# Optimization experiments

Hardware: AMD Instinct MI355X
Metric: run time of the kernel (lower is better)

## Reference

```python
import jax, jax.numpy as jnp
import numpy as np

H = 8          # num_heads (in_channels > 8)
BN_EPS = 1e-5  # torch BatchNorm2d default


def _l2norm(w):
    # torch.norm(w, 2, dim=-2, keepdim=True) + 1e-4
    return jnp.sqrt(jnp.sum(w * w, axis=-2, keepdims=True)) + 1e-4


def setup_inputs() -> dict:
    key = jax.random.key(0)
    ks = jax.random.split(key, 6)
    N, C, T, V = 64, 128, 128, 25
    x = jax.random.normal(ks[0], (N, C, T, V), dtype=jnp.float32)
    fc1 = jax.random.normal(ks[1], (3, H, V, V), dtype=jnp.float32)
    rpe = jax.random.normal(ks[2], (3, H, V), dtype=jnp.float32)
    hops = jax.random.randint(ks[3], (V, V), 0, V)
    fc2_w = jax.random.normal(ks[4], (3, C, C // H), dtype=jnp.float32) * 0.1
    fc2_b = jax.random.normal(ks[5], (3, C), dtype=jnp.float32) * 0.1
    gamma = jnp.ones((C,), dtype=jnp.float32)
    beta = jnp.zeros((C,), dtype=jnp.float32)
    return {"x": x, "fc1": fc1, "rpe": rpe, "hops": hops,
            "fc2_w": fc2_w, "fc2_b": fc2_b, "gamma": gamma, "beta": beta}


def reference(x, fc1, rpe, hops, fc2_w, fc2_b, gamma, beta):
    N, C, T, V = x.shape
    c = C // H
    # relative-position embedding gathered by hop distance: (3, H, V, V)
    pos_emb = rpe[:, :, hops]
    x_in = x.reshape(N, H, c, T, V)
    y = jnp.zeros((N, H, c, T, V), dtype=x.dtype)
    for i in range(3):
        # normalized adaptive adjacency + normalized positional term
        w1 = fc1[i] / _l2norm(fc1[i]) + pos_emb[i] / _l2norm(pos_emb[i])  # (H, V, V)
        z = jnp.einsum('nhctv,hvw->nhctw', x_in, w1)
        # grouped 1x1 conv == per-head channel mixing
        wg = fc2_w[i].reshape(H, c, c)                       # (H, out_per_group, in_per_group)
        z = jnp.einsum('nhctv,hdc->nhdtv', z, wg)
        z = z + fc2_b[i].reshape(1, H, c, 1, 1)
        y = y + z
    y = y.reshape(N, C, T, V)
    # BatchNorm2d (training-mode batch statistics, biased variance)
    mean = jnp.mean(y, axis=(0, 2, 3), keepdims=True)
    var = jnp.var(y, axis=(0, 2, 3), keepdims=True)
    y = gamma.reshape(1, C, 1, 1) * (y - mean) * jax.lax.rsqrt(var + BN_EPS) + beta.reshape(1, C, 1, 1)
    # residual (in_channels == out_channels -> identity down) + ReLU
    return jax.nn.relu(y + x)
```

## Files before the change

### kernel.cpp

```cpp
#include <hip/hip_runtime.h>
#include <hip/hip_bf16.h>

namespace {

constexpr int kN = 64, kC = 128, kT = 128, kV = 25, kH = 8, kc = 16;
constexpr int kKS = 13;
constexpr int kBCol = 448;
constexpr int kBStep = kBCol * 32;
constexpr int kXRow = 424;

typedef __attribute__((ext_vector_type(8))) short bf16x8;
typedef __attribute__((ext_vector_type(8))) unsigned short u16x8;
typedef __attribute__((ext_vector_type(4))) float f32x4;

__device__ inline unsigned short f2bf(float f) {
    unsigned int u = __builtin_bit_cast(unsigned int, f);
    u += 0x7fffu + ((u >> 16) & 1u);
    return (unsigned short)(u >> 16);
}

__device__ inline float bf2f(unsigned short s) {
    return __builtin_bit_cast(float, ((unsigned int)s) << 16);
}

__device__ inline void glds16(const void* g, void* l) {
    __builtin_amdgcn_global_load_lds(
        (const __attribute__((address_space(1))) void*)g,
        (__attribute__((address_space(3))) void*)l, 16, 0, 0);
}
__device__ inline void glds4(const void* g, void* l) {
    __builtin_amdgcn_global_load_lds(
        (const __attribute__((address_space(1))) void*)g,
        (__attribute__((address_space(3))) void*)l, 4, 0, 0);
}

#define VMWAIT(n) do { asm volatile("s_waitcnt vmcnt(" #n ")" ::: "memory"); \
                       __builtin_amdgcn_sched_barrier(0); } while (0)
#define LGKM0     do { asm volatile("s_waitcnt lgkmcnt(0)" ::: "memory"); \
                       __builtin_amdgcn_sched_barrier(0); } while (0)
#define BAR()     __builtin_amdgcn_s_barrier()

__global__ void precompute_w1(const float* __restrict__ fc1,
                              const float* __restrict__ rpe,
                              const int* __restrict__ hops,
                              float* __restrict__ W1) {
    int ih = blockIdx.x;
    int w = threadIdx.x;
    if (w >= kV) return;
    const float* f = fc1 + ih * kV * kV;
    const float* r = rpe + ih * kV;
    float s1 = 0.f, s2 = 0.f;
    for (int v = 0; v < kV; ++v) {
        float a = f[v * kV + w];
        float p = r[hops[v * kV + w]];
        s1 += a * a; s2 += p * p;
    }
    float n1 = sqrtf(s1) + 1e-4f, n2 = sqrtf(s2) + 1e-4f;
    float* o = W1 + ih * kV * kV;
    for (int v = 0; v < kV; ++v) {
        float a = f[v * kV + w];
        float p = r[hops[v * kV + w]];
        o[v * kV + w] = a / n1 + p / n2;
    }
}

__global__ void precompute_W(const float* __restrict__ W1,
                             const float* __restrict__ fc2_w,
                             unsigned short* __restrict__ Wt3) {
    int k = blockIdx.x;
    int h = blockIdx.y;
    unsigned short* outp = Wt3 + ((size_t)h * kKS + k) * kBStep;
    for (int e = threadIdx.x; e < kBStep; e += 256) {
        int col = e >> 5, lo = e & 31;
        int kap = k * 32 + lo;
        int c = kap / 26, vv = kap - c * 26;
        float val = 0.f;
        if (vv < 25 && col < 400) {
            int d = col / 25, w = col - d * 25;
            #pragma unroll
            for (int i = 0; i < 3; ++i) {
                float wg = fc2_w[(i * kC + h * kc + d) * kc + c];
                float w1 = W1[((i * kH + h) * kV + vv) * kV + w];
                val += wg * w1;
            }
        }
        outp[e] = f2bf(val);
    }
}

__global__ __launch_bounds__(256, 1) void gemm_y(const float* __restrict__ x,
                                                 const unsigned short* __restrict__ Wt3,
                                                 unsigned short* __restrict__ yb) {
    __shared__ __align__(16) unsigned short Xl[64 * kXRow];
    __shared__ __align__(16) unsigned short Bl[2][kBStep];

    const int n = blockIdx.x, tb = blockIdx.y, h = blockIdx.z;
    const int tid = threadIdx.x, lane = tid & 63, wv = tid >> 6;
    const int ll = lane & 15, lh = lane >> 4;
    const int t0 = tb * 64;

    const float* xbase = x + ((size_t)(n * kC + h * kc) * kT + t0) * kV;
    const unsigned short* bbase = Wt3 + (size_t)h * kKS * kBStep;

    auto stage_x = [&](int s, int buf) {
        float* bb = (float*)&Bl[buf][0];
        const float* src0 = xbase + (size_t)(s * 4) * (kT * kV);
        #pragma unroll
        for (int q = 0; q < 25; ++q) {
            int e = q * 256 + tid;
            int c = e / 1600, off = e - c * 1600;
            glds4(src0 + (size_t)c * (kT * kV) + off, bb + e);
        }
    };
    auto convert = [&](int s, int buf) {
        const float* bp = (const float*)&Bl[buf][0] + (tid & 3) * 1600 + (tid >> 2) * 25;
        unsigned int* xw = (unsigned int*)&Xl[(size_t)(tid >> 2) * kXRow + (s * 4 + (tid & 3)) * 26];
        #pragma unroll
        for (int p = 0; p < 13; ++p) {
            float f0 = bp[2 * p];
            float f1 = (p < 12) ? bp[2 * p + 1] : 0.f;
            xw[p] = (unsigned)f2bf(f0) | ((unsigned)f2bf(f1) << 16);
        }
    };
    auto stage_b = [&](int k, int buf) {
        const unsigned short* src = bbase + (size_t)k * kBStep;
        unsigned short* dst = &Bl[buf][0];
        #pragma unroll
        for (int q = 0; q < 7; ++q)
            glds16(src + (size_t)(q * 256 + tid) * 8, dst + (size_t)(q * 256 + tid) * 8);
    };

    stage_x(0, 0); stage_x(1, 1);
    VMWAIT(25); BAR();
    convert(0, 0);
    LGKM0; BAR();
    stage_x(2, 0);
    VMWAIT(25); BAR();
    convert(1, 1);
    LGKM0; BAR();
    stage_x(3, 1);
    VMWAIT(25); BAR();
    convert(2, 0);
    LGKM0; BAR();
    stage_b(0, 0);
    VMWAIT(7); BAR();
    convert(3, 1);
    LGKM0; BAR();

    f32x4 acc[4][7];
    #pragma unroll
    for (int a = 0; a < 4; ++a)
        #pragma unroll
        for (int b = 0; b < 7; ++b) acc[a][b] = (f32x4)(0.f);

    for (int k = 0; k < kKS; ++k) {
        const int cur = k & 1;
        if (k < kKS - 1) {
            stage_b(k + 1, cur ^ 1);
            VMWAIT(7);
        } else {
            VMWAIT(0);
        }
        BAR();

        bf16x8 af0 = *(const bf16x8*)&Xl[(size_t)((0 * 16 + ll) * kXRow) + k * 32 + lh * 8];
        bf16x8 af1 = *(const bf16x8*)&Xl[(size_t)((1 * 16 + ll) * kXRow) + k * 32 + lh * 8];
        bf16x8 af2 = *(const bf16x8*)&Xl[(size_t)((2 * 16 + ll) * kXRow) + k * 32 + lh * 8];
        bf16x8 af3 = *(const bf16x8*)&Xl[(size_t)((3 * 16 + ll) * kXRow) + k * 32 + lh * 8];
        #pragma unroll
        for (int ci = 0; ci < 7; ++ci) {
            bf16x8 bf = *(const bf16x8*)&Bl[cur][(size_t)(((wv * 7 + ci) * 16 + ll) * 32) + lh * 8];
            acc[0][ci] = __builtin_amdgcn_mfma_f32_16x16x32_bf16(af0, bf, acc[0][ci], 0, 0, 0);
            acc[1][ci] = __builtin_amdgcn_mfma_f32_16x16x32_bf16(af1, bf, acc[1][ci], 0, 0, 0);
            acc[2][ci] = __builtin_amdgcn_mfma_f32_16x16x32_bf16(af2, bf, acc[2][ci], 0, 0, 0);
            acc[3][ci] = __builtin_amdgcn_mfma_f32_16x16x32_bf16(af3, bf, acc[3][ci], 0, 0, 0);
        }
        BAR();
    }

    #pragma unroll
    for (int rf = 0; rf < 4; ++rf) {
        int t = t0 + rf * 16 + lh * 4;
        #pragma unroll
        for (int ci = 0; ci < 7; ++ci) {
            int m = (wv * 7 + ci) * 16 + ll;
            if (m < 400) {
                int d = m / 25, w = m - d * 25;
                unsigned short* yp = yb + ((size_t)(n * kC + h * kc + d) * kT + t) * kV + w;
                #pragma unroll
                for (int r = 0; r < 4; ++r)
                    yp[(size_t)r * kV] = f2bf(acc[rf][ci][r]);
            }
        }
    }
}

__global__ void bn_partial(const unsigned short* __restrict__ yb,
                           float2* __restrict__ partials) {
    int g  = blockIdx.x;
    int ch = blockIdx.y;
    int tid = threadIdx.x;
    float s = 0.f, ss = 0.f;
    for (int n = g * 8; n < g * 8 + 8; ++n) {
        const u16x8* p = (const u16x8*)(yb + (size_t)(n * kC + ch) * (kT * kV));
        for (int e = tid; e < 400; e += 256) {
            u16x8 v = p[e];
            #pragma unroll
            for (int j = 0; j < 8; ++j) {
                float f = bf2f((unsigned short)v[j]);
                s += f; ss += f * f;
            }
        }
    }
    __shared__ float rs[256], rss[256];
    rs[tid] = s; rss[tid] = ss;
    __syncthreads();
    for (int o = 128; o > 0; o >>= 1) {
        if (tid < o) { rs[tid] += rs[tid + o]; rss[tid] += rss[tid + o]; }
        __syncthreads();
    }
    if (tid == 0) partials[ch * 8 + g] = make_float2(rs[0], rss[0]);
}

__global__ void bn_finalize(const float2* __restrict__ partials,
                            const float* __restrict__ gamma,
                            const float* __restrict__ beta,
                            float2* __restrict__ scsh) {
    int ch = threadIdx.x;
    if (ch >= kC) return;
    float s = 0.f, ss = 0.f;
    for (int g = 0; g < 8; ++g) {
        float2 p = partials[ch * 8 + g];
        s += p.x; ss += p.y;
    }
    const float inv = 1.f / (float)(kN * kT * kV);
    float mean = s * inv;
    float var  = ss * inv - mean * mean;
    float sc = gamma[ch] * rsqrtf(var + 1e-5f);
    scsh[ch] = make_float2(sc, beta[ch] - mean * sc);
}

__global__ void bn_apply(const unsigned short* __restrict__ yb,
                         const float* __restrict__ x,
                         const float2* __restrict__ scsh,
                         float* __restrict__ out) {
    const size_t total8 = (size_t)kN * kC * kT * kV / 8;
    for (size_t i = (size_t)blockIdx.x * blockDim.x + threadIdx.x; i < total8;
         i += (size_t)gridDim.x * blockDim.x) {
        int ch = (int)((i / 400) % kC);
        float2 sc = scsh[ch];
        u16x8 yv = ((const u16x8*)yb)[i];
        f32x4 x0 = ((const f32x4*)x)[i * 2];
        f32x4 x1 = ((const f32x4*)x)[i * 2 + 1];
        f32x4 o0, o1;
        #pragma unroll
        for (int q = 0; q < 4; ++q) {
            o0[q] = fmaxf(bf2f((unsigned short)yv[q]) * sc.x + sc.y + x0[q], 0.f);
            o1[q] = fmaxf(bf2f((unsigned short)yv[q + 4]) * sc.x + sc.y + x1[q], 0.f);
        }
        ((f32x4*)out)[i * 2]     = o0;
        ((f32x4*)out)[i * 2 + 1] = o1;
    }
}

}

extern "C" void kernel_launch(void* const* d_in, const int* in_sizes, int n_in,
                              void* d_out, int out_size, void* d_ws, size_t ws_size,
                              hipStream_t stream) {
    const float* x     = (const float*)d_in[0];
    const float* fc1   = (const float*)d_in[1];
    const float* rpe   = (const float*)d_in[2];
    const int*   hops  = (const int*)d_in[3];
    const float* fc2w  = (const float*)d_in[4];
    const float* gamma = (const float*)d_in[6];
    const float* beta  = (const float*)d_in[7];
    float* out = (float*)d_out;

    char* ws = (char*)d_ws;
    unsigned short* yb       = (unsigned short*)ws;
    float*          W1       = (float*)(ws + 52428800);
    unsigned short* Wt3      = (unsigned short*)(ws + 52494336);
    float2*         partials = (float2*)(ws + 55476224);
    float2*         scsh     = (float2*)(ws + 55484416);

    precompute_w1<<<24, 32, 0, stream>>>(fc1, rpe, hops, W1);
    precompute_W<<<dim3(13, 8), 256, 0, stream>>>(W1, fc2w, Wt3);
    gemm_y<<<dim3(64, 2, 8), 256, 0, stream>>>(x, Wt3, yb);
    bn_partial<<<dim3(8, 128), 256, 0, stream>>>(yb, partials);
    bn_finalize<<<1, 128, 0, stream>>>(partials, gamma, beta, scsh);
    bn_apply<<<2048, 256, 0, stream>>>(yb, x, scsh, out);
}
```

Measured before the change: 160.8 us.

## Fuse BN partial statistics into GEMM epilogue and single-buffer LDS for occupancy

Computes per-channel sum and sum-of-squares from the fp32 accumulators inside the GEMM kernel, reduces them through shuffles and LDS, and writes per-block partials. This removes the separate bn_partial kernel and its full re-read of the bf16 intermediate. The B staging buffer is also cut to a single buffer and launch bounds are raised to 2 blocks per CU. X staging now uses 16-byte loads and a rotated convert order to reduce bank conflicts. The costs are that double-buffered prefetch overlap is lost and the statistics are taken from fp32 values rather than the rounded bf16 ones.

After: 131.3 us. 1.22x faster.

```diff
diff --git a/kernel.cpp b/kernel.cpp
--- a/kernel.cpp
+++ b/kernel.cpp
@@ -7,7 +7,7 @@
 constexpr int kKS = 13;
 constexpr int kBCol = 448;
 constexpr int kBStep = kBCol * 32;
-constexpr int kXRow = 424;
+constexpr int kXRow = 416;
 
 typedef __attribute__((ext_vector_type(8))) short bf16x8;
 typedef __attribute__((ext_vector_type(8))) unsigned short u16x8;
@@ -18,25 +18,18 @@
     u += 0x7fffu + ((u >> 16) & 1u);
     return (unsigned short)(u >> 16);
 }
-
 __device__ inline float bf2f(unsigned short s) {
     return __builtin_bit_cast(float, ((unsigned int)s) << 16);
 }
-
 __device__ inline void glds16(const void* g, void* l) {
     __builtin_amdgcn_global_load_lds(
         (const __attribute__((address_space(1))) void*)g,
         (__attribute__((address_space(3))) void*)l, 16, 0, 0);
 }
-__device__ inline void glds4(const void* g, void* l) {
-    __builtin_amdgcn_global_load_lds(
-        (const __attribute__((address_space(1))) void*)g,
-        (__attribute__((address_space(3))) void*)l, 4, 0, 0);
-}
-
-#define VMWAIT(n) do { asm volatile("s_waitcnt vmcnt(" #n ")" ::: "memory"); \
+
+#define VMWAIT0() do { asm volatile("s_waitcnt vmcnt(0)" ::: "memory"); \
                        __builtin_amdgcn_sched_barrier(0); } while (0)
-#define LGKM0     do { asm volatile("s_waitcnt lgkmcnt(0)" ::: "memory"); \
+#define LGKM0()   do { asm volatile("s_waitcnt lgkmcnt(0)" ::: "memory"); \
                        __builtin_amdgcn_sched_barrier(0); } while (0)
 #define BAR()     __builtin_amdgcn_s_barrier()
 
@@ -88,64 +81,63 @@
     }
 }
 
-__global__ __launch_bounds__(256, 1) void gemm_y(const float* __restrict__ x,
+__global__ __launch_bounds__(256, 2) void gemm_y(const float* __restrict__ x,
                                                  const unsigned short* __restrict__ Wt3,
-                                                 unsigned short* __restrict__ yb) {
+                                                 unsigned short* __restrict__ yb,
+                                                 float2* __restrict__ Pbuf) {
     __shared__ __align__(16) unsigned short Xl[64 * kXRow];
-    __shared__ __align__(16) unsigned short Bl[2][kBStep];
-
-    const int n = blockIdx.x, tb = blockIdx.y, h = blockIdx.z;
+    __shared__ __align__(16) unsigned short Bl[kBStep];
+
+    const int tb = blockIdx.x, n = blockIdx.y, h = blockIdx.z;
     const int tid = threadIdx.x, lane = tid & 63, wv = tid >> 6;
     const int ll = lane & 15, lh = lane >> 4;
     const int t0 = tb * 64;
 
     const float* xbase = x + ((size_t)(n * kC + h * kc) * kT + t0) * kV;
     const unsigned short* bbase = Wt3 + (size_t)h * kKS * kBStep;
-
-    auto stage_x = [&](int s, int buf) {
-        float* bb = (float*)&Bl[buf][0];
-        const float* src0 = xbase + (size_t)(s * 4) * (kT * kV);
-        #pragma unroll
-        for (int q = 0; q < 25; ++q) {
+    float* Blf = (float*)&Bl[0];
+
+    auto stage_x = [&](int s) {
+        #pragma unroll
+        for (int q = 0; q < 7; ++q) {
             int e = q * 256 + tid;
-            int c = e / 1600, off = e - c * 1600;
-            glds4(src0 + (size_t)c * (kT * kV) + off, bb + e);
+            if (e < 1600) {
+                int c = e / 400, off = e - c * 400;
+                glds16(xbase + (size_t)(s * 4 + c) * 3200 + off * 4,
+                       (char*)Bl + (size_t)e * 16);
+            }
         }
     };
-    auto convert = [&](int s, int buf) {
-        const float* bp = (const float*)&Bl[buf][0] + (tid & 3) * 1600 + (tid >> 2) * 25;
-        unsigned int* xw = (unsigned int*)&Xl[(size_t)(tid >> 2) * kXRow + (s * 4 + (tid & 3)) * 26];
-        #pragma unroll
-        for (int p = 0; p < 13; ++p) {
+    auto stage_b = [&](int k) {
+        const unsigned short* src = bbase + (size_t)k * kBStep;
+        #pragma unroll
+        for (int q = 0; q < 7; ++q) {
+            int e = q * 256 + tid;
+            glds16(src + (size_t)e * 8, Bl + (size_t)e * 8);
+        }
+    };
+    auto convert = [&](int s) {
+        const int t = lane;
+        const int t13 = t % 13;
+        const float* bp = Blf + wv * 1600 + t * 25;
+        unsigned int* xw = (unsigned int*)&Xl[0] + t * (kXRow / 2) + (s * 4 + wv) * 13;
+        #pragma unroll
+        for (int i = 0; i < 13; ++i) {
+            int p = i + t13; if (p >= 13) p -= 13;
             float f0 = bp[2 * p];
             float f1 = (p < 12) ? bp[2 * p + 1] : 0.f;
             xw[p] = (unsigned)f2bf(f0) | ((unsigned)f2bf(f1) << 16);
         }
     };
-    auto stage_b = [&](int k, int buf) {
-        const unsigned short* src = bbase + (size_t)k * kBStep;
-        unsigned short* dst = &Bl[buf][0];
-        #pragma unroll
-        for (int q = 0; q < 7; ++q)
-            glds16(src + (size_t)(q * 256 + tid) * 8, dst + (size_t)(q * 256 + tid) * 8);
-    };
-
-    stage_x(0, 0); stage_x(1, 1);
-    VMWAIT(25); BAR();
-    convert(0, 0);
-    LGKM0; BAR();
-    stage_x(2, 0);
-    VMWAIT(25); BAR();
-    convert(1, 1);
-    LGKM0; BAR();
-    stage_x(3, 1);
-    VMWAIT(25); BAR();
-    convert(2, 0);
-    LGKM0; BAR();
-    stage_b(0, 0);
-    VMWAIT(7); BAR();
-    convert(3, 1);
-    LGKM0; BAR();
+
+    #pragma unroll 1
+    for (int s = 0; s < 4; ++s) {
+        stage_x(s);
+        VMWAIT0(); BAR();
+        convert(s);
+        LGKM0(); BAR();
+    }
+    stage_b(0);
 
     f32x4 acc[4][7];
     #pragma unroll
@@ -153,29 +145,30 @@
         #pragma unroll
         for (int b = 0; b < 7; ++b) acc[a][b] = (f32x4)(0.f);
 
+    #pragma unroll 1
     for (int k = 0; k < kKS; ++k) {
-        const int cur = k & 1;
-        if (k < kKS - 1) {
-            stage_b(k + 1, cur ^ 1);
-            VMWAIT(7);
-        } else {
-            VMWAIT(0);
-        }
+        VMWAIT0();
         BAR();
 
-        bf16x8 af0 = *(const bf16x8*)&Xl[(size_t)((0 * 16 + ll) * kXRow) + k * 32 + lh * 8];
-        bf16x8 af1 = *(const bf16x8*)&Xl[(size_t)((1 * 16 + ll) * kXRow) + k * 32 + lh * 8];
-        bf16x8 af2 = *(const bf16x8*)&Xl[(size_t)((2 * 16 + ll) * kXRow) + k * 32 + lh * 8];
-        bf16x8 af3 = *(const bf16x8*)&Xl[(size_t)((3 * 16 + ll) * kXRow) + k * 32 + lh * 8];
+        bf16x8 a0 = *(const bf16x8*)&Xl[(size_t)(0 * 16 + ll) * kXRow + k * 32 + lh * 8];
+        bf16x8 a1 = *(const bf16x8*)&Xl[(size_t)(1 * 16 + ll) * kXRow + k * 32 + lh * 8];
+        bf16x8 a2 = *(const bf16x8*)&Xl[(size_t)(2 * 16 + ll) * kXRow + k * 32 + lh * 8];
+        bf16x8 a3 = *(const bf16x8*)&Xl[(size_t)(3 * 16 + ll) * kXRow + k * 32 + lh * 8];
+        bf16x8 b[7];
+        #pragma unroll
+        for (int ci = 0; ci < 7; ++ci)
+            b[ci] = *(const bf16x8*)&Bl[(size_t)((wv * 7 + ci) * 16 + ll) * 32 + lh * 8];
+
+        LGKM0(); BAR();
+        if (k < kKS - 1) stage_b(k + 1);
+
         #pragma unroll
         for (int ci = 0; ci < 7; ++ci) {
-            bf16x8 bf = *(const bf16x8*)&Bl[cur][(size_t)(((wv * 7 + ci) * 16 + ll) * 32) + lh * 8];
-            acc[0][ci] = __builtin_amdgcn_mfma_f32_16x16x32_bf16(af0, bf, acc[0][ci], 0, 0, 0);
-            acc[1][ci] = __builtin_amdgcn_mfma_f32_16x16x32_bf16(af1, bf, acc[1][ci], 0, 0, 0);
-            acc[2][ci] = __builtin_amdgcn_mfma_f32_16x16x32_bf16(af2, bf, acc[2][ci], 0, 0, 0);
-            acc[3][ci] = __builtin_amdgcn_mfma_f32_16x16x32_bf16(af3, bf, acc[3][ci], 0, 0, 0);
-        }
-        BAR();
+            acc[0][ci] = __builtin_amdgcn_mfma_f32_16x16x32_bf16(a0, b[ci], acc[0][ci], 0, 0, 0);
+            acc[1][ci] = __builtin_amdgcn_mfma_f32_16x16x32_bf16(a1, b[ci], acc[1][ci], 0, 0, 0);
+            acc[2][ci] = __builtin_amdgcn_mfma_f32_16x16x32_bf16(a2, b[ci], acc[2][ci], 0, 0, 0);
+            acc[3][ci] = __builtin_amdgcn_mfma_f32_16x16x32_bf16(a3, b[ci], acc[3][ci], 0, 0, 0);
+        }
     }
 
     #pragma unroll
@@ -183,7 +176,7 @@
         int t = t0 + rf * 16 + lh * 4;
         #pragma unroll
         for (int ci = 0; ci < 7; ++ci) {
-            int m = (wv * 7 + ci) * 16 + ll;
+            int m = wv * 112 + ci * 16 + ll;
             if (m < 400) {
                 int d = m / 25, w = m - d * 25;
                 unsigned short* yp = yb + ((size_t)(n * kC + h * kc + d) * kT + t) * kV + w;
@@ -193,44 +186,44 @@
             }
         }
     }
-}
-
-__global__ void bn_partial(const unsigned short* __restrict__ yb,
-                           float2* __restrict__ partials) {
-    int g  = blockIdx.x;
-    int ch = blockIdx.y;
-    int tid = threadIdx.x;
-    float s = 0.f, ss = 0.f;
-    for (int n = g * 8; n < g * 8 + 8; ++n) {
-        const u16x8* p = (const u16x8*)(yb + (size_t)(n * kC + ch) * (kT * kV));
-        for (int e = tid; e < 400; e += 256) {
-            u16x8 v = p[e];
+
+    float2* Bs = (float2*)&Bl[0];
+    #pragma unroll
+    for (int ci = 0; ci < 7; ++ci) {
+        float s = 0.f, ss = 0.f;
+        #pragma unroll
+        for (int rf = 0; rf < 4; ++rf)
             #pragma unroll
-            for (int j = 0; j < 8; ++j) {
-                float f = bf2f((unsigned short)v[j]);
-                s += f; ss += f * f;
-            }
-        }
-    }
-    __shared__ float rs[256], rss[256];
-    rs[tid] = s; rss[tid] = ss;
+            for (int r = 0; r < 4; ++r) {
+                float v = acc[rf][ci][r];
+                s += v; ss += v * v;
+            }
+        s  += __shfl_xor(s, 16);  ss += __shfl_xor(ss, 16);
+        s  += __shfl_xor(s, 32);  ss += __shfl_xor(ss, 32);
+        if (lh == 0) Bs[wv * 112 + ci * 16 + ll] = make_float2(s, ss);
+    }
     __syncthreads();
-    for (int o = 128; o > 0; o >>= 1) {
-        if (tid < o) { rs[tid] += rs[tid + o]; rss[tid] += rss[tid + o]; }
-        __syncthreads();
-    }
-    if (tid == 0) partials[ch * 8 + g] = make_float2(rs[0], rss[0]);
-}
-
-__global__ void bn_finalize(const float2* __restrict__ partials,
+    if (tid < 16) {
+        float s = 0.f, ss = 0.f;
+        for (int w = 0; w < 25; ++w) {
+            float2 p = Bs[tid * 25 + w];
+            s += p.x; ss += p.y;
+        }
+        size_t bid = (size_t)tb + 2 * ((size_t)n + 64 * (size_t)h);
+        Pbuf[bid * 16 + tid] = make_float2(s, ss);
+    }
+}
+
+__global__ void bn_finalize(const float2* __restrict__ Pbuf,
                             const float* __restrict__ gamma,
                             const float* __restrict__ beta,
                             float2* __restrict__ scsh) {
     int ch = threadIdx.x;
     if (ch >= kC) return;
+    int h = ch >> 4, d = ch & 15;
     float s = 0.f, ss = 0.f;
-    for (int g = 0; g < 8; ++g) {
-        float2 p = partials[ch * 8 + g];
+    for (int j = 0; j < 128; ++j) {
+        float2 p = Pbuf[(size_t)(j + 128 * h) * 16 + d];
         s += p.x; ss += p.y;
     }
     const float inv = 1.f / (float)(kN * kT * kV);
@@ -278,16 +271,15 @@
     float* out = (float*)d_out;
 
     char* ws = (char*)d_ws;
-    unsigned short* yb       = (unsigned short*)ws;
-    float*          W1       = (float*)(ws + 52428800);
-    unsigned short* Wt3      = (unsigned short*)(ws + 52494336);
-    float2*         partials = (float2*)(ws + 55476224);
-    float2*         scsh     = (float2*)(ws + 55484416);
+    unsigned short* yb   = (unsigned short*)ws;
+    float*          W1   = (float*)(ws + 52428800);
+    unsigned short* Wt3  = (unsigned short*)(ws + 52494336);
+    float2*         Pbuf = (float2*)(ws + 55476224);
+    float2*         scsh = (float2*)(ws + 55607296);
 
     precompute_w1<<<24, 32, 0, stream>>>(fc1, rpe, hops, W1);
     precompute_W<<<dim3(13, 8), 256, 0, stream>>>(W1, fc2w, Wt3);
-    gemm_y<<<dim3(64, 2, 8), 256, 0, stream>>>(x, Wt3, yb);
-    bn_partial<<<dim3(8, 128), 256, 0, stream>>>(yb, partials);
-    bn_finalize<<<1, 128, 0, stream>>>(partials, gamma, beta, scsh);
+    gemm_y<<<dim3(2, 64, 8), 256, 0, stream>>>(x, Wt3, yb, Pbuf);
+    bn_finalize<<<1, 128, 0, stream>>>(Pbuf, gamma, beta, scsh);
     bn_apply<<<2048, 256, 0, stream>>>(yb, x, scsh, out);
 }
```
